# Kernel optimization log

Measured on AMD Instinct MI355X. Metric: run time of the kernel, lower is better.

The kernel has to match this reference:

```python
import jax, jax.numpy as jnp
import numpy as np

B, T, D, K, NF = 4, 1024, 1024, 4, 4
MAXD = 256          # TemporalEncoding max_delta
NC = 32             # ConceptGraph n_concepts
LN_EPS = 1e-5


def setup_inputs() -> dict:
    key = jax.random.key(0)
    ks = jax.random.split(key, 12)
    s = 0.02  # weight init scale
    return {
        "x": jax.random.normal(ks[0], (B, T, D), jnp.float32),
        "routed_tokens": jax.random.normal(ks[1], (B, T, K, D), jnp.float32),
        "sim": jax.random.normal(ks[2], (B, T, K), jnp.float32),
        # per-function logic Linear(3D->D), LayerNorm(D), gate Linear(3D->D)
        "Wl": jax.random.normal(ks[3], (NF, 3 * D, D), jnp.float32) * s,
        "bl": jnp.zeros((NF, D), jnp.float32),
        "ln_g": jnp.ones((NF, D), jnp.float32),
        "ln_b": jnp.zeros((NF, D), jnp.float32),
        "Wg": jax.random.normal(ks[4], (NF, 3 * D, D), jnp.float32) * s,
        "bg": jnp.zeros((NF, D), jnp.float32),
        # fn_selector Linear(D -> NF)
        "Wsel": jax.random.normal(ks[5], (D, NF), jnp.float32) * s,
        "bsel": jnp.zeros((NF,), jnp.float32),
        # temporal embedding table [2*max_delta+1, D]
        "delta_table": jax.random.normal(ks[6], (2 * MAXD + 1, D), jnp.float32) * s,
        # VQ codebook (ConceptGraph.embedding buffer)
        "codebook": jax.random.normal(ks[7], (NC, D), jnp.float32),
        "topk_indices": jax.random.randint(ks[8], (B, T, K), 0, T),
    }


def reference(x, routed_tokens, sim, Wl, bl, ln_g, ln_b, Wg, bg,
              Wsel, bsel, delta_table, codebook, topk_indices):
    Bx, Tx, Dx = x.shape
    Kx = routed_tokens.shape[2]
    N = Bx * Tx

    # temporal encoding: delta = t - topk_index, clamped into table range
    t = jnp.arange(Tx)[None, :, None]
    idx = jnp.clip(t - topk_indices + MAXD, 0, 2 * MAXD)
    de = delta_table[idx].reshape(N, Kx, Dx)            # [N,K,D]

    xf = x.reshape(N, Dx)
    rf = routed_tokens.reshape(N, Kx, Dx)
    sf = sim.reshape(N, Kx)

    tok = jnp.broadcast_to(xf[:, None, :], (N, Kx, Dx))
    comb = jnp.concatenate([tok, rf, de], axis=-1)       # [N,K,3D]

    # all NF reasoning functions at once: logic MLP + GELU + LayerNorm
    h = jnp.einsum('nkc,fcd->fnkd', comb, Wl) + bl[:, None, None, :]
    h = jax.nn.gelu(h, approximate=False)
    mu = jnp.mean(h, axis=-1, keepdims=True)
    var = jnp.var(h, axis=-1, keepdims=True)
    h = (h - mu) / jnp.sqrt(var + LN_EPS)
    h = h * ln_g[:, None, None, :] + ln_b[:, None, None, :]  # [F,N,K,D]

    sw = jax.nn.softmax(sf, axis=-1)                     # [N,K]
    arg = jnp.einsum('nk,fnkd->fnd', sw, h)              # [F,N,D]

    tok_f = jnp.broadcast_to(xf[None], (Wl.shape[0], N, Dx))
    gin = jnp.concatenate([tok_f, arg, arg], axis=-1)    # [F,N,3D]
    gate = jax.nn.sigmoid(jnp.einsum('fnc,fcd->fnd', gin, Wg) + bg[:, None, :])

    fw = jax.nn.softmax(xf @ Wsel + bsel, axis=-1)       # [N,F]
    proposed = jnp.einsum('nf,fnd->nd', fw, arg)
    gsum = jnp.einsum('nf,fnd->nd', fw, gate)
    uf = proposed * gsum                                 # [N,D] updated tokens

    # ConceptGraph VQ (eval: no EMA update): pairwise dist, argmin, gather
    d2 = (jnp.sum(uf * uf, axis=1, keepdims=True)
          - 2.0 * uf @ codebook.T
          + jnp.sum(codebook * codebook, axis=1))        # [N,NC]
    enc = jnp.argmin(d2, axis=1)                         # [N]
    quant = codebook[enc]                                # [N,D]
    out = uf + jax.lax.stop_gradient(quant - uf)         # straight-through
    return out.reshape(Bx, Tx, Dx)
```

## Files before the change

### kernel.cpp

```cpp
#include <hip/hip_runtime.h>
#include <hip/hip_bf16.h>
#include <cmath>


typedef __bf16 bf16x8 __attribute__((ext_vector_type(8)));
typedef float  f32x4  __attribute__((ext_vector_type(4)));

__device__ __forceinline__ float gelu_f(float v) {
    return 0.5f * v * (1.0f + erff(v * 0.7071067811865476f));
}

__device__ __forceinline__ void split8(const float* v, bf16x8& H, bf16x8& L) {
#pragma unroll
    for (int j = 0; j < 8; ++j) {
        float x = v[j];
        __bf16 h = (__bf16)x;
        H[j] = h;
        L[j] = (__bf16)(x - (float)h);
    }
}

#define GLL16(src, dst)                                                        \
    __builtin_amdgcn_global_load_lds(                                          \
        (const __attribute__((address_space(1))) void*)(src),                  \
        (__attribute__((address_space(3))) void*)(dst), 16, 0, 0)

#define SWZ_DECODE()                                                           \
    int bx, by, bz;                                                            \
    {                                                                          \
        const int nx = gridDim.x, ny = gridDim.y;                              \
        const int nwg = nx * ny * (int)gridDim.z;                              \
        const int bid = blockIdx.x + nx * (blockIdx.y + ny * blockIdx.z);      \
        const int q = nwg >> 3;                                                \
        const int rm = (bid & 7) * q + (bid >> 3);                             \
        bx = rm % nx; by = (rm / nx) % ny; bz = rm / (nx * ny);                \
    }

#define STAGE_WRITE()                                                          \
    _Pragma("unroll")                                                          \
    for (int i = 0; i < 4; ++i) {                                              \
        int u = tid + i * 256;                                                 \
        int arow = u >> 3, ag = u & 7;                                         \
        bf16x8 H, L; split8(ra[i], H, L);                                      \
        char* dst = lds + arow * 128 + ((ag ^ (arow & 7)) << 4);               \
        *(bf16x8*)dst = H; *(bf16x8*)(dst + 16384) = L;                        \
    }                                                                          \
    _Pragma("unroll")                                                          \
    for (int i = 0; i < 4; ++i) {                                              \
        int u = tid + i * 256;                                                 \
        int bcol = u & 127, bgu = u >> 7;                                      \
        bf16x8 H, L; split8(rb[i], H, L);                                      \
        char* dst = lds + 32768 + bcol * 128 + ((bgu ^ (bcol & 7)) << 4);      \
        *(bf16x8*)dst = H; *(bf16x8*)(dst + 16384) = L;                        \
    }

#define MFMA64()                                                               \
    _Pragma("unroll")                                                          \
    for (int ks = 0; ks < 2; ++ks) {                                           \
        bf16x8 ah[4], al[4], bh[4], bl_[4];                                    \
        _Pragma("unroll")                                                      \
        for (int mi = 0; mi < 4; ++mi) {                                       \
            const char* pa = lds + (wr + mi * 16 + rl) * 128                   \
                             + (((ks * 4 + g) ^ (rl & 7)) << 4);               \
            ah[mi] = *(const bf16x8*)pa;                                       \
            al[mi] = *(const bf16x8*)(pa + 16384);                             \
        }                                                                      \
        _Pragma("unroll")                                                      \
        for (int ni = 0; ni < 4; ++ni) {                                       \
            const char* pb = lds + 32768 + (wc + ni * 16 + rl) * 128           \
                             + (((ks * 4 + g) ^ (rl & 7)) << 4);               \
            bh[ni]  = *(const bf16x8*)pb;                                      \
            bl_[ni] = *(const bf16x8*)(pb + 16384);                            \
        }                                                                      \
        _Pragma("unroll")                                                      \
        for (int mi = 0; mi < 4; ++mi)                                         \
            _Pragma("unroll")                                                  \
            for (int ni = 0; ni < 4; ++ni) {                                   \
                acc[mi][ni] = __builtin_amdgcn_mfma_f32_16x16x32_bf16(ah[mi], bh[ni],  acc[mi][ni], 0, 0, 0); \
                acc[mi][ni] = __builtin_amdgcn_mfma_f32_16x16x32_bf16(ah[mi], bl_[ni], acc[mi][ni], 0, 0, 0); \
                acc[mi][ni] = __builtin_amdgcn_mfma_f32_16x16x32_bf16(al[mi], bh[ni],  acc[mi][ni], 0, 0, 0); \
            }                                                                  \
    }

__global__ __launch_bounds__(256, 2) void gemm64(
    const float* __restrict__ A, int arowBase, int maxrow,
    const float* __restrict__ B, int kbase,
    float* __restrict__ C, int nkt,
    size_t bStrideZ, size_t cStrideZ, int mrows)
{
    __shared__ __align__(16) char lds[65536];
    const int tid = threadIdx.x, wid = tid >> 6, lane = tid & 63;
    SWZ_DECODE();
    const int bm0 = bx * 128, bn0 = by * 128;
    const float* Bf = B + bz * bStrideZ;
    float* Cp = C + bz * cStrideZ;
    const int wr = (wid >> 1) * 64, wc = (wid & 1) * 64;
    const int g = lane >> 4, rl = lane & 15;

    float ra[4][8], rb[4][8];

#define LOADA64(KC0)                                                           \
    _Pragma("unroll")                                                          \
    for (int i = 0; i < 4; ++i) {                                              \
        int u = tid + i * 256;                                                 \
        int r = arowBase + bm0 + (u >> 3); if (r > maxrow) r = maxrow;         \
        const float* s = A + (size_t)r * 1024 + (KC0) + (u & 7) * 8;           \
        *(float4*)&ra[i][0] = ((const float4*)s)[0];                           \
        *(float4*)&ra[i][4] = ((const float4*)s)[1];                           \
    }
#define LOADB64(KC0)                                                           \
    _Pragma("unroll")                                                          \
    for (int i = 0; i < 4; ++i) {                                              \
        int u = tid + i * 256;                                                 \
        int bcol = bn0 + (u & 127);                                            \
        int k0 = kbase + (KC0) + (u >> 7) * 8;                                 \
        _Pragma("unroll")                                                      \
        for (int j = 0; j < 8; ++j)                                            \
            rb[i][j] = Bf[(size_t)(k0 + j) * 1024 + bcol];                     \
    }

    f32x4 acc[4][4];
    f32x4 zero = {0.f, 0.f, 0.f, 0.f};
#pragma unroll
    for (int i = 0; i < 4; ++i)
#pragma unroll
        for (int j = 0; j < 4; ++j) acc[i][j] = zero;

    LOADA64(0) LOADB64(0)
    for (int kt = 0; kt < nkt; ++kt) {
        STAGE_WRITE()
        __syncthreads();
        if (kt + 1 < nkt) { LOADA64((kt + 1) * 64) LOADB64((kt + 1) * 64) }
        MFMA64()
        __syncthreads();
    }
#undef LOADA64
#undef LOADB64

    const int cg = lane & 15, rg = (lane >> 4) * 4;
#pragma unroll
    for (int mi = 0; mi < 4; ++mi) {
#pragma unroll
        for (int i = 0; i < 4; ++i) {
            int row_out = bm0 + wr + mi * 16 + rg + i;
            if (row_out >= mrows) continue;
#pragma unroll
            for (int ni = 0; ni < 4; ++ni) {
                int col = bn0 + wc + ni * 16 + cg;
                Cp[(size_t)row_out * 1024 + col] = acc[mi][ni][i];
            }
        }
    }
}

__global__ __launch_bounds__(256) void precvt_wg(
    const float* __restrict__ Wg, char* __restrict__ img)
{
    const int u = blockIdx.x * 256 + threadIdx.x;
    const int col = u & 127;
    const int kt  = (u >> 7) & 63;
    const int ct  = (u >> 13) & 7;
    const int f   = u >> 16;
    const int colg = ct * 128 + col;
    const float* Wf = Wg + (size_t)f * 3072 * 1024;
    const bool sum2 = (kt >= 32);

    float vv[32];
#pragma unroll
    for (int j = 0; j < 32; ++j) {
        int k = kt * 32 + j;
        float v = Wf[(size_t)k * 1024 + colg];
        if (sum2) v += Wf[(size_t)(k + 1024) * 1024 + colg];
        vv[j] = v;
    }
    char* tb = img + ((((size_t)f * 8 + ct) * 64) + kt) * 16384;
    const int swz = (col >> 1) & 3;
#pragma unroll
    for (int g = 0; g < 4; ++g) {
        bf16x8 H, L; split8(&vv[g * 8], H, L);
        char* dst = tb + col * 64 + ((g ^ swz) << 4);
        *(bf16x8*)dst = H;
        *(bf16x8*)(dst + 8192) = L;
    }
}

__global__ __launch_bounds__(256, 3) void gate_bimg(
    const float* __restrict__ x, const float* __restrict__ arg,
    const char* __restrict__ img, const float* __restrict__ fw,
    const float* __restrict__ bg, float* __restrict__ g2, int fbase)
{
    __shared__ __align__(16) char lds[49152];
    const int tid = threadIdx.x, wid = tid >> 6, lane = tid & 63;
    SWZ_DECODE();
    const int bm0 = bx * 128, bn0 = by * 128;
    const int z = bz, f = fbase + z;
    const float* argf = arg + (size_t)f * 4096 * 1024;
    const char* Bt = img + (((size_t)f * 8 + by) * 64) * 16384;
    const int wr = (wid >> 1) * 64, wc = (wid & 1) * 64;
    const int g = lane >> 4, rl = lane & 15;
    const int goff = ((g ^ ((rl >> 1) & 3)) << 4);
    const int boff = wid * 4096 + lane * 16;

    float ra[2][8];

#define LOADA_G(KT)                                                            \
    _Pragma("unroll")                                                          \
    for (int i = 0; i < 2; ++i) {                                              \
        int u = tid + i * 256;                                                 \
        int r = bm0 + (u >> 2);                                                \
        int k0 = (KT) * 32 + (u & 3) * 8;                                      \
        const float* s = (k0 < 1024) ? (x + (size_t)r * 1024 + k0)             \
                                     : (argf + (size_t)r * 1024 + (k0 - 1024));\
        *(float4*)&ra[i][0] = ((const float4*)s)[0];                           \
        *(float4*)&ra[i][4] = ((const float4*)s)[1];                           \
    }
#define LOADB_G(KT, BUF)                                                       \
    {                                                                          \
        const char* sb = Bt + (size_t)(KT) * 16384 + boff;                     \
        char* db = lds + 16384 + (BUF) * 16384 + boff;                         \
        GLL16(sb,        db);                                                  \
        GLL16(sb + 1024, db + 1024);                                           \
        GLL16(sb + 2048, db + 2048);                                           \
        GLL16(sb + 3072, db + 3072);                                           \
    }

    f32x4 acc[4][4];
    f32x4 zero = {0.f, 0.f, 0.f, 0.f};
#pragma unroll
    for (int i = 0; i < 4; ++i)
#pragma unroll
        for (int j = 0; j < 4; ++j) acc[i][j] = zero;

    LOADA_G(0)
    LOADB_G(0, 0)
    for (int kt = 0; kt < 64; ++kt) {
        __syncthreads();
#pragma unroll
        for (int i = 0; i < 2; ++i) {
            int u = tid + i * 256;
            int row = u >> 2, ag = u & 3;
            bf16x8 H, L; split8(ra[i], H, L);
            char* dst = lds + row * 64 + ((ag ^ ((row >> 1) & 3)) << 4);
            *(bf16x8*)dst = H;
            *(bf16x8*)(dst + 8192) = L;
        }
        __syncthreads();
        if (kt + 1 < 64) {
            LOADB_G(kt + 1, (kt + 1) & 1)
            LOADA_G(kt + 1)
        }
        {
            const char* LDSA = lds;
            const char* LDSB = lds + 16384 + (kt & 1) * 16384;
            bf16x8 ah[4], al[4], bh[4], bl_[4];
#pragma unroll
            for (int mi = 0; mi < 4; ++mi) {
                const char* pa = LDSA + (wr + mi * 16 + rl) * 64 + goff;
                ah[mi] = *(const bf16x8*)pa;
                al[mi] = *(const bf16x8*)(pa + 8192);
            }
#pragma unroll
            for (int ni = 0; ni < 4; ++ni) {
                const char* pb = LDSB + (wc + ni * 16 + rl) * 64 + goff;
                bh[ni]  = *(const bf16x8*)pb;
                bl_[ni] = *(const bf16x8*)(pb + 8192);
            }
#pragma unroll
            for (int mi = 0; mi < 4; ++mi)
#pragma unroll
                for (int ni = 0; ni < 4; ++ni) {
                    acc[mi][ni] = __builtin_amdgcn_mfma_f32_16x16x32_bf16(ah[mi], bh[ni],  acc[mi][ni], 0, 0, 0);
                    acc[mi][ni] = __builtin_amdgcn_mfma_f32_16x16x32_bf16(ah[mi], bl_[ni], acc[mi][ni], 0, 0, 0);
                    acc[mi][ni] = __builtin_amdgcn_mfma_f32_16x16x32_bf16(al[mi], bh[ni],  acc[mi][ni], 0, 0, 0);
                }
        }
    }
#undef LOADA_G
#undef LOADB_G

    const int cg = lane & 15, rg = (lane >> 4) * 4;
    const bool accum = (fbase > 0);
#pragma unroll
    for (int mi = 0; mi < 4; ++mi) {
#pragma unroll
        for (int i = 0; i < 4; ++i) {
            int row_out = bm0 + wr + mi * 16 + rg + i;
            float fwv = fw[(size_t)row_out * 4 + f];
#pragma unroll
            for (int ni = 0; ni < 4; ++ni) {
                int col = bn0 + wc + ni * 16 + cg;
                float v = acc[mi][ni][i] + bg[f * 1024 + col];
                float s = fwv / (1.0f + expf(-v));
                size_t off = ((size_t)z * 4096 + row_out) * 1024 + col;
                if (accum) g2[off] += s; else g2[off] = s;
            }
        }
    }
}

__global__ __launch_bounds__(256) void fw_kernel(
    const float* __restrict__ x, const float* __restrict__ Wsel,
    const float* __restrict__ bsel, float* __restrict__ fw)
{
    __shared__ float sred[16];
    const int n = blockIdx.x;
    const int tid = threadIdx.x, w = tid >> 6, lane = tid & 63;

    float4 xv = *(const float4*)&x[(size_t)n * 1024 + tid * 4];
    float pf0 = 0, pf1 = 0, pf2 = 0, pf3 = 0;
    const float* wrp = &Wsel[(size_t)tid * 16];
    pf0 += xv.x * wrp[0];  pf1 += xv.x * wrp[1];  pf2 += xv.x * wrp[2];  pf3 += xv.x * wrp[3];
    pf0 += xv.y * wrp[4];  pf1 += xv.y * wrp[5];  pf2 += xv.y * wrp[6];  pf3 += xv.y * wrp[7];
    pf0 += xv.z * wrp[8];  pf1 += xv.z * wrp[9];  pf2 += xv.z * wrp[10]; pf3 += xv.z * wrp[11];
    pf0 += xv.w * wrp[12]; pf1 += xv.w * wrp[13]; pf2 += xv.w * wrp[14]; pf3 += xv.w * wrp[15];
    for (int o = 32; o; o >>= 1) {
        pf0 += __shfl_xor(pf0, o); pf1 += __shfl_xor(pf1, o);
        pf2 += __shfl_xor(pf2, o); pf3 += __shfl_xor(pf3, o);
    }
    if (lane == 0) { sred[w*4+0] = pf0; sred[w*4+1] = pf1; sred[w*4+2] = pf2; sred[w*4+3] = pf3; }
    __syncthreads();
    if (tid == 0) {
        float s0 = sred[0] + sred[4] + sred[8]  + sred[12] + bsel[0];
        float s1 = sred[1] + sred[5] + sred[9]  + sred[13] + bsel[1];
        float s2 = sred[2] + sred[6] + sred[10] + sred[14] + bsel[2];
        float s3 = sred[3] + sred[7] + sred[11] + sred[15] + bsel[3];
        float mx = fmaxf(fmaxf(s0, s1), fmaxf(s2, s3));
        float e0 = expf(s0 - mx), e1 = expf(s1 - mx), e2 = expf(s2 - mx), e3 = expf(s3 - mx);
        float inv = 1.0f / (e0 + e1 + e2 + e3);
        float4 o = { e0 * inv, e1 * inv, e2 * inv, e3 * inv };
        *(float4*)&fw[(size_t)n * 4] = o;
    }
}

__global__ __launch_bounds__(256) void ln_fuse_kernel(
    const float* __restrict__ hpre, const float* __restrict__ de_proj,
    const float* __restrict__ bl, const float* __restrict__ ln_g,
    const float* __restrict__ ln_b, const float* __restrict__ sim,
    const int* __restrict__ topk, float* __restrict__ arg,
    int f, int token_base, const float* __restrict__ xl)
{
    __shared__ float red[4 * 1024];
    const int n = token_base + blockIdx.x;
    const int k = threadIdx.x >> 6, lane = threadIdx.x & 63;
    const float* hrow = hpre + ((size_t)blockIdx.x * 4 + k) * 1024;
    const int t  = n & 1023;
    const int tk = topk[(size_t)n * 4 + k];
    int di = t - tk + 256; di = di < 0 ? 0 : (di > 512 ? 512 : di);
    const float* drow = de_proj + ((size_t)f * 513 + di) * 1024;
    const float* blr = bl + f * 1024;
    const float* gr  = ln_g + f * 1024;
    const float* br  = ln_b + f * 1024;
    const float* xr  = xl + (size_t)n * 1024;

    float4 s4 = *(const float4*)&sim[(size_t)n * 4];
    float smax = fmaxf(fmaxf(s4.x, s4.y), fmaxf(s4.z, s4.w));
    float e0 = expf(s4.x - smax), e1 = expf(s4.y - smax);
    float e2 = expf(s4.z - smax), e3 = expf(s4.w - smax);
    float swk = (k == 0 ? e0 : k == 1 ? e1 : k == 2 ? e2 : e3) / (e0 + e1 + e2 + e3);

    float gv[16];
    float ssum = 0.f;
#pragma unroll
    for (int j = 0; j < 4; ++j) {
        int d4 = lane + j * 64;
        float4 h  = *(const float4*)&hrow[d4 * 4];
        float4 dd = *(const float4*)&drow[d4 * 4];
        float4 bb = *(const float4*)&blr[d4 * 4];
        float4 xv = *(const float4*)&xr[d4 * 4];
        float a0 = gelu_f(h.x + xv.x + dd.x + bb.x);
        float a1 = gelu_f(h.y + xv.y + dd.y + bb.y);
        float a2 = gelu_f(h.z + xv.z + dd.z + bb.z);
        float a3 = gelu_f(h.w + xv.w + dd.w + bb.w);
        gv[j*4+0] = a0; gv[j*4+1] = a1; gv[j*4+2] = a2; gv[j*4+3] = a3;
        ssum += a0 + a1 + a2 + a3;
    }
    for (int o = 32; o; o >>= 1) ssum += __shfl_xor(ssum, o);
    float mu = ssum * 0.0009765625f;
    float vs = 0.f;
#pragma unroll
    for (int i = 0; i < 16; ++i) { float dm = gv[i] - mu; vs += dm * dm; }
    for (int o = 32; o; o >>= 1) vs += __shfl_xor(vs, o);
    float rstd = 1.0f / sqrtf(vs * 0.0009765625f + 1e-5f);
#pragma unroll
    for (int j = 0; j < 4; ++j) {
        int d4 = lane + j * 64;
        float4 g4 = *(const float4*)&gr[d4 * 4];
        float4 b4 = *(const float4*)&br[d4 * 4];
        float4 y;
        y.x = ((gv[j*4+0] - mu) * rstd * g4.x + b4.x) * swk;
        y.y = ((gv[j*4+1] - mu) * rstd * g4.y + b4.y) * swk;
        y.z = ((gv[j*4+2] - mu) * rstd * g4.z + b4.z) * swk;
        y.w = ((gv[j*4+3] - mu) * rstd * g4.w + b4.w) * swk;
        *(float4*)&red[k * 1024 + d4 * 4] = y;
    }
    __syncthreads();
    const int p = threadIdx.x;
    float4 r0 = *(const float4*)&red[0 * 1024 + p * 4];
    float4 r1 = *(const float4*)&red[1 * 1024 + p * 4];
    float4 r2 = *(const float4*)&red[2 * 1024 + p * 4];
    float4 r3 = *(const float4*)&red[3 * 1024 + p * 4];
    float4 o;
    o.x = r0.x + r1.x + r2.x + r3.x;
    o.y = r0.y + r1.y + r2.y + r3.y;
    o.z = r0.z + r1.z + r2.z + r3.z;
    o.w = r0.w + r1.w + r2.w + r3.w;
    *(float4*)&arg[((size_t)f * 4096 + n) * 1024 + p * 4] = o;
}

__global__ __launch_bounds__(256) void final_kernel(
    const float* __restrict__ fw, const float* __restrict__ arg,
    const float* __restrict__ g2, const float* __restrict__ cb,
    float* __restrict__ out)
{
    __shared__ float uf_s[1024];
    __shared__ float score_s[32];
    __shared__ int enc_s;
    const int n = blockIdx.x;
    const int tid = threadIdx.x, w = tid >> 6, lane = tid & 63;

    float4 fwv = *(const float4*)&fw[(size_t)n * 4];
    float fwa[4] = { fwv.x, fwv.y, fwv.z, fwv.w };

    float4 prop = {0, 0, 0, 0};
#pragma unroll
    for (int f = 0; f < 4; ++f) {
        float4 av = *(const float4*)&arg[((size_t)f * 4096 + n) * 1024 + tid * 4];
        prop.x += fwa[f] * av.x; prop.y += fwa[f] * av.y;
        prop.z += fwa[f] * av.z; prop.w += fwa[f] * av.w;
    }
    float4 ga = *(const float4*)&g2[(size_t)n * 1024 + tid * 4];
    float4 gb = *(const float4*)&g2[(size_t)(4096 + n) * 1024 + tid * 4];
    float4 uf;
    uf.x = prop.x * (ga.x + gb.x); uf.y = prop.y * (ga.y + gb.y);
    uf.z = prop.z * (ga.z + gb.z); uf.w = prop.w * (ga.w + gb.w);
    *(float4*)&uf_s[tid * 4] = uf;
    __syncthreads();

#pragma unroll
    for (int cc = 0; cc < 8; ++cc) {
        int c = w * 8 + cc;
        float p = 0.f, q = 0.f;
#pragma unroll
        for (int j = 0; j < 4; ++j) {
            int d4 = lane + j * 64;
            float4 u4 = *(const float4*)&uf_s[d4 * 4];
            float4 c4 = *(const float4*)&cb[(size_t)c * 1024 + d4 * 4];
            p += u4.x * c4.x + u4.y * c4.y + u4.z * c4.z + u4.w * c4.w;
            q += c4.x * c4.x + c4.y * c4.y + c4.z * c4.z + c4.w * c4.w;
        }
        float s = q - 2.0f * p;
        for (int o = 32; o; o >>= 1) s += __shfl_xor(s, o);
        if (lane == 0) score_s[c] = s;
    }
    __syncthreads();
    if (tid < 64) {
        float v; int idx;
        if (lane < 32) { v = score_s[lane]; idx = lane; }
        else           { v = INFINITY;      idx = 1 << 30; }
        for (int o = 16; o; o >>= 1) {
            float ov = __shfl_xor(v, o); int oi = __shfl_xor(idx, o);
            if (ov < v || (ov == v && oi < idx)) { v = ov; idx = oi; }
        }
        if (lane == 0) enc_s = idx;
    }
    __syncthreads();
    const int enc = enc_s;
    float4 o4 = *(const float4*)&cb[(size_t)enc * 1024 + tid * 4];
    *(float4*)&out[(size_t)n * 1024 + tid * 4] = o4;
}

extern "C" void kernel_launch(void* const* d_in, const int* in_sizes, int n_in,
                              void* d_out, int out_size, void* d_ws, size_t ws_size,
                              hipStream_t stream)
{
    const float* x    = (const float*)d_in[0];
    const float* rf   = (const float*)d_in[1];
    const float* sim  = (const float*)d_in[2];
    const float* Wl   = (const float*)d_in[3];
    const float* bl   = (const float*)d_in[4];
    const float* ln_g = (const float*)d_in[5];
    const float* ln_b = (const float*)d_in[6];
    const float* Wg   = (const float*)d_in[7];
    const float* bg   = (const float*)d_in[8];
    const float* Wsel = (const float*)d_in[9];
    const float* bsel = (const float*)d_in[10];
    const float* dtab = (const float*)d_in[11];
    const float* cb   = (const float*)d_in[12];
    const int*   topk = (const int*)d_in[13];
    float* out = (float*)d_out;
    dim3 blk(256);

    const size_t NEED = 142622720ull;
    if (ws_size < NEED) return;
    char* ws = (char*)d_ws;
    float* arg     = (float*)(ws + 0);
    float* de_proj = (float*)(ws + 67108864);
    float* xl2     = (float*)(ws + 75513856);
    float* hbuf    = (float*)(ws + 109068288);
    char*  Wgimg   = ws + 67108864;
    float* g2      = (float*)(ws + 100663296);
    float* fw      = (float*)(ws + 134217728);

    gemm64<<<dim3(5, 8, 4), blk, 0, stream>>>(
        dtab, 0, 512, Wl, 2048, de_proj, 16,
        (size_t)3072 * 1024, (size_t)513 * 1024, 513);

    for (int pair = 0; pair < 2; ++pair) {
        gemm64<<<dim3(32, 8, 2), blk, 0, stream>>>(
            x, 0, 4095, Wl + (size_t)pair * 2 * 3072 * 1024, 0, xl2, 16,
            (size_t)3072 * 1024, (size_t)4096 * 1024, 4096);
        for (int fi = 0; fi < 2; ++fi) {
            int f = pair * 2 + fi;
            const float* Wlf = Wl + (size_t)f * 3072 * 1024;
            const float* xlf = xl2 + (size_t)fi * 4096 * 1024;
            for (int ch = 0; ch < 2; ++ch) {
                gemm64<<<dim3(64, 8, 1), blk, 0, stream>>>(
                    rf, ch * 8192, 16383, Wlf, 1024, hbuf, 16, 0, 0, 8192);
                ln_fuse_kernel<<<2048, blk, 0, stream>>>(
                    hbuf, de_proj, bl, ln_g, ln_b, sim, topk, arg,
                    f, ch * 2048, xlf);
            }
        }
    }

    precvt_wg<<<1024, blk, 0, stream>>>(Wg, Wgimg);

    fw_kernel<<<4096, blk, 0, stream>>>(x, Wsel, bsel, fw);

    gate_bimg<<<dim3(32, 8, 2), blk, 0, stream>>>(x, arg, Wgimg, fw, bg, g2, 0);
    gate_bimg<<<dim3(32, 8, 2), blk, 0, stream>>>(x, arg, Wgimg, fw, bg, g2, 2);

    final_kernel<<<4096, blk, 0, stream>>>(fw, arg, g2, cb, out);
}
```

Measured before the change: 1.094 ms.

## Pre-split routed-token weights into bf16 image and double-buffer LDS in GEMMs

The routed-token GEMM now reads a precomputed hi/lo bf16 image of the Wl middle slice, loaded with global_load_lds, instead of strided fp32 B loads split into bf16 on every tile. The gate GEMM and the new routed GEMM use double-buffered A and B LDS stages with one barrier per k-step. The x projection for all four functions is done in one launch written into the arg buffer, which lets ln_fuse read and overwrite in place. The goal is to cut B-operand conversion work and barrier stalls, at the cost of an extra conversion pass and workspace aliasing between xl and arg.

Result: faster. 1.012 ms (-7.5%).

```diff
diff --git a/kernel.cpp b/kernel.cpp
--- a/kernel.cpp
+++ b/kernel.cpp
@@ -36,12 +36,238 @@
         bx = rm % nx; by = (rm / nx) % ny; bz = rm / (nx * ny);                \
     }
 
-#define STAGE_WRITE()                                                          \
+__global__ __launch_bounds__(256) void precvt_img(
+    const float* __restrict__ W, char* __restrict__ img,
+    int krowBase, int nktLog, int sumFromKt)
+{
+    const int u = blockIdx.x * 256 + threadIdx.x;
+    const int col = u & 127;
+    const int kt  = (u >> 7) & ((1 << nktLog) - 1);
+    const int ct  = (u >> (7 + nktLog)) & 7;
+    const int f   = u >> (10 + nktLog);
+    const int colg = ct * 128 + col;
+    const float* Wf = W + (size_t)f * 3072 * 1024;
+    const bool sum2 = (kt >= sumFromKt);
+
+    float vv[32];
+#pragma unroll
+    for (int j = 0; j < 32; ++j) {
+        int k = krowBase + kt * 32 + j;
+        float v = Wf[(size_t)k * 1024 + colg];
+        if (sum2) v += Wf[(size_t)(k + 1024) * 1024 + colg];
+        vv[j] = v;
+    }
+    char* tb = img + ((((size_t)f * 8 + ct) << nktLog) + kt) * 16384;
+    const int swz = (col >> 1) & 3;
+#pragma unroll
+    for (int g = 0; g < 4; ++g) {
+        bf16x8 H, L; split8(&vv[g * 8], H, L);
+        char* dst = tb + col * 64 + ((g ^ swz) << 4);
+        *(bf16x8*)dst = H;
+        *(bf16x8*)(dst + 8192) = L;
+    }
+}
+
+#define WRITEA_SPLIT(AB)                                                       \
+    {                                                                          \
+        int row = tid >> 2, ag = tid & 3;                                      \
+        bf16x8 H, L; split8(ra[0], H, L);                                      \
+        char* d = (AB) + row * 64 + ((ag ^ ((row >> 1) & 3)) << 4);            \
+        *(bf16x8*)d = H; *(bf16x8*)(d + 8192) = L;                             \
+        int row2 = row + 64;                                                   \
+        split8(ra[1], H, L);                                                   \
+        char* d2 = (AB) + row2 * 64 + ((ag ^ ((row2 >> 1) & 3)) << 4);         \
+        *(bf16x8*)d2 = H; *(bf16x8*)(d2 + 8192) = L;                           \
+    }
+
+#define LOADB_IMG(KT, BB)                                                      \
+    {                                                                          \
+        const char* sb = Bt + (size_t)(KT) * 16384 + boff;                     \
+        char* db = (BB) + boff;                                                \
+        GLL16(sb,        db);                                                  \
+        GLL16(sb + 1024, db + 1024);                                           \
+        GLL16(sb + 2048, db + 2048);                                           \
+        GLL16(sb + 3072, db + 3072);                                           \
+    }
+
+#define MFMA32(AB, BB)                                                         \
+    {                                                                          \
+        bf16x8 ah[4], al[4], bh[4], bl_[4];                                    \
+        _Pragma("unroll")                                                      \
+        for (int mi = 0; mi < 4; ++mi) {                                       \
+            const char* pa = (AB) + (wr + mi * 16 + rl) * 64 + goff;           \
+            ah[mi] = *(const bf16x8*)pa;                                       \
+            al[mi] = *(const bf16x8*)(pa + 8192);                              \
+        }                                                                      \
+        _Pragma("unroll")                                                      \
+        for (int ni = 0; ni < 4; ++ni) {                                       \
+            const char* pb = (BB) + (wc + ni * 16 + rl) * 64 + goff;           \
+            bh[ni]  = *(const bf16x8*)pb;                                      \
+            bl_[ni] = *(const bf16x8*)(pb + 8192);                             \
+        }                                                                      \
+        _Pragma("unroll")                                                      \
+        for (int mi = 0; mi < 4; ++mi)                                         \
+            _Pragma("unroll")                                                  \
+            for (int ni = 0; ni < 4; ++ni) {                                   \
+                acc[mi][ni] = __builtin_amdgcn_mfma_f32_16x16x32_bf16(ah[mi], bh[ni],  acc[mi][ni], 0, 0, 0); \
+                acc[mi][ni] = __builtin_amdgcn_mfma_f32_16x16x32_bf16(ah[mi], bl_[ni], acc[mi][ni], 0, 0, 0); \
+                acc[mi][ni] = __builtin_amdgcn_mfma_f32_16x16x32_bf16(al[mi], bh[ni],  acc[mi][ni], 0, 0, 0); \
+            }                                                                  \
+    }
+
+__global__ __launch_bounds__(256, 2) void himg(
+    const float* __restrict__ rfA, int rowBase,
+    const char* __restrict__ img, int fimg,
+    float* __restrict__ hbuf)
+{
+    __shared__ __align__(16) char lds[65536];
+    const int tid = threadIdx.x, wid = tid >> 6, lane = tid & 63;
+    SWZ_DECODE();
+    (void)bz;
+    const int bm0 = bx * 128, bn0 = by * 128;
+    const char* Bt = img + (size_t)((fimg * 8 + by) << 5) * 16384;
+    const int wr = (wid >> 1) * 64, wc = (wid & 1) * 64;
+    const int g = lane >> 4, rl = lane & 15;
+    const int goff = ((g ^ ((rl >> 1) & 3)) << 4);
+    const int boff = wid * 4096 + lane * 16;
+    char* A0 = lds;            char* A1 = lds + 16384;
+    char* B0 = lds + 32768;    char* B1 = lds + 49152;
+
+    const float* abase = rfA + (size_t)(rowBase + bm0 + (tid >> 2)) * 1024 + (tid & 3) * 8;
+    float ra[2][8];
+#define LOADA_H(KT)                                                            \
+    {                                                                          \
+        const float* s = abase + (KT) * 32;                                    \
+        *(float4*)&ra[0][0] = ((const float4*)s)[0];                           \
+        *(float4*)&ra[0][4] = ((const float4*)s)[1];                           \
+        const float* s2 = s + 64 * 1024;                                       \
+        *(float4*)&ra[1][0] = ((const float4*)s2)[0];                          \
+        *(float4*)&ra[1][4] = ((const float4*)s2)[1];                          \
+    }
+
+    f32x4 acc[4][4];
+    f32x4 zero = {0.f, 0.f, 0.f, 0.f};
+#pragma unroll
+    for (int i = 0; i < 4; ++i)
+#pragma unroll
+        for (int j = 0; j < 4; ++j) acc[i][j] = zero;
+
+    LOADA_H(0)
+    LOADB_IMG(0, B0)
+    WRITEA_SPLIT(A0)
+    LOADA_H(1)
+    __syncthreads();
+    for (int kt = 0; kt < 32; ++kt) {
+        char* Ac = (kt & 1) ? A1 : A0;  char* Bc = (kt & 1) ? B1 : B0;
+        char* An = (kt & 1) ? A0 : A1;  char* Bn = (kt & 1) ? B0 : B1;
+        if (kt < 31) {
+            LOADB_IMG(kt + 1, Bn)
+            WRITEA_SPLIT(An)
+            if (kt < 30) LOADA_H(kt + 2)
+        }
+        MFMA32(Ac, Bc)
+        __syncthreads();
+    }
+#undef LOADA_H
+
+    const int cg = lane & 15, rg = (lane >> 4) * 4;
+#pragma unroll
+    for (int mi = 0; mi < 4; ++mi)
+#pragma unroll
+        for (int i = 0; i < 4; ++i) {
+            int row_out = bm0 + wr + mi * 16 + rg + i;
+#pragma unroll
+            for (int ni = 0; ni < 4; ++ni) {
+                int col = bn0 + wc + ni * 16 + cg;
+                hbuf[(size_t)row_out * 1024 + col] = acc[mi][ni][i];
+            }
+        }
+}
+
+__global__ __launch_bounds__(256, 2) void gate_img(
+    const float* __restrict__ x, const float* __restrict__ arg,
+    const char* __restrict__ img, const float* __restrict__ fw,
+    const float* __restrict__ bg, float* __restrict__ g2, int fbase)
+{
+    __shared__ __align__(16) char lds[65536];
+    const int tid = threadIdx.x, wid = tid >> 6, lane = tid & 63;
+    SWZ_DECODE();
+    const int bm0 = bx * 128, bn0 = by * 128;
+    const int z = bz, f = fbase + z;
+    const float* argf = arg + (size_t)f * 4096 * 1024;
+    const char* Bt = img + (size_t)((f * 8 + by) << 6) * 16384;
+    const int wr = (wid >> 1) * 64, wc = (wid & 1) * 64;
+    const int g = lane >> 4, rl = lane & 15;
+    const int goff = ((g ^ ((rl >> 1) & 3)) << 4);
+    const int boff = wid * 4096 + lane * 16;
+    char* A0 = lds;            char* A1 = lds + 16384;
+    char* B0 = lds + 32768;    char* B1 = lds + 49152;
+
+    const int arow = bm0 + (tid >> 2);
+    const int akc  = (tid & 3) * 8;
+    float ra[2][8];
+#define LOADA_G(KT)                                                            \
+    {                                                                          \
+        int k0 = (KT) * 32 + akc;                                              \
+        const float* base = (k0 < 1024) ? x : (argf - 1024);                   \
+        const float* s  = base + (size_t)arow * 1024 + k0;                     \
+        const float* s2 = base + (size_t)(arow + 64) * 1024 + k0;              \
+        *(float4*)&ra[0][0] = ((const float4*)s)[0];                           \
+        *(float4*)&ra[0][4] = ((const float4*)s)[1];                           \
+        *(float4*)&ra[1][0] = ((const float4*)s2)[0];                          \
+        *(float4*)&ra[1][4] = ((const float4*)s2)[1];                          \
+    }
+
+    f32x4 acc[4][4];
+    f32x4 zero = {0.f, 0.f, 0.f, 0.f};
+#pragma unroll
+    for (int i = 0; i < 4; ++i)
+#pragma unroll
+        for (int j = 0; j < 4; ++j) acc[i][j] = zero;
+
+    LOADA_G(0)
+    LOADB_IMG(0, B0)
+    WRITEA_SPLIT(A0)
+    LOADA_G(1)
+    __syncthreads();
+    for (int kt = 0; kt < 64; ++kt) {
+        char* Ac = (kt & 1) ? A1 : A0;  char* Bc = (kt & 1) ? B1 : B0;
+        char* An = (kt & 1) ? A0 : A1;  char* Bn = (kt & 1) ? B0 : B1;
+        if (kt < 63) {
+            LOADB_IMG(kt + 1, Bn)
+            WRITEA_SPLIT(An)
+            if (kt < 62) LOADA_G(kt + 2)
+        }
+        MFMA32(Ac, Bc)
+        __syncthreads();
+    }
+#undef LOADA_G
+
+    const int cg = lane & 15, rg = (lane >> 4) * 4;
+    const bool accum = (fbase > 0);
+#pragma unroll
+    for (int mi = 0; mi < 4; ++mi)
+#pragma unroll
+        for (int i = 0; i < 4; ++i) {
+            int row_out = bm0 + wr + mi * 16 + rg + i;
+            float fwv = fw[(size_t)row_out * 4 + f];
+#pragma unroll
+            for (int ni = 0; ni < 4; ++ni) {
+                int col = bn0 + wc + ni * 16 + cg;
+                float v = acc[mi][ni][i] + bg[f * 1024 + col];
+                float s = fwv / (1.0f + expf(-v));
+                size_t off = ((size_t)z * 4096 + row_out) * 1024 + col;
+                if (accum) g2[off] += s; else g2[off] = s;
+            }
+        }
+}
+
+#define STAGE_WRITE64()                                                        \
     _Pragma("unroll")                                                          \
     for (int i = 0; i < 4; ++i) {                                              \
         int u = tid + i * 256;                                                 \
         int arow = u >> 3, ag = u & 7;                                         \
-        bf16x8 H, L; split8(ra[i], H, L);                                      \
+        bf16x8 H, L; split8(rav[i], H, L);                                     \
         char* dst = lds + arow * 128 + ((ag ^ (arow & 7)) << 4);               \
         *(bf16x8*)dst = H; *(bf16x8*)(dst + 16384) = L;                        \
     }                                                                          \
@@ -49,7 +275,7 @@
     for (int i = 0; i < 4; ++i) {                                              \
         int u = tid + i * 256;                                                 \
         int bcol = u & 127, bgu = u >> 7;                                      \
-        bf16x8 H, L; split8(rb[i], H, L);                                      \
+        bf16x8 H, L; split8(rbv[i], H, L);                                     \
         char* dst = lds + 32768 + bcol * 128 + ((bgu ^ (bcol & 7)) << 4);      \
         *(bf16x8*)dst = H; *(bf16x8*)(dst + 16384) = L;                        \
     }
@@ -97,7 +323,7 @@
     const int wr = (wid >> 1) * 64, wc = (wid & 1) * 64;
     const int g = lane >> 4, rl = lane & 15;
 
-    float ra[4][8], rb[4][8];
+    float rav[4][8], rbv[4][8];
 
 #define LOADA64(KC0)                                                           \
     _Pragma("unroll")                                                          \
@@ -105,8 +331,8 @@
         int u = tid + i * 256;                                                 \
         int r = arowBase + bm0 + (u >> 3); if (r > maxrow) r = maxrow;         \
         const float* s = A + (size_t)r * 1024 + (KC0) + (u & 7) * 8;           \
-        *(float4*)&ra[i][0] = ((const float4*)s)[0];                           \
-        *(float4*)&ra[i][4] = ((const float4*)s)[1];                           \
+        *(float4*)&rav[i][0] = ((const float4*)s)[0];                          \
+        *(float4*)&rav[i][4] = ((const float4*)s)[1];                          \
     }
 #define LOADB64(KC0)                                                           \
     _Pragma("unroll")                                                          \
@@ -116,7 +342,7 @@
         int k0 = kbase + (KC0) + (u >> 7) * 8;                                 \
         _Pragma("unroll")                                                      \
         for (int j = 0; j < 8; ++j)                                            \
-            rb[i][j] = Bf[(size_t)(k0 + j) * 1024 + bcol];                     \
+            rbv[i][j] = Bf[(size_t)(k0 + j) * 1024 + bcol];                    \
     }
 
     f32x4 acc[4][4];
@@ -128,7 +354,7 @@
 
     LOADA64(0) LOADB64(0)
     for (int kt = 0; kt < nkt; ++kt) {
-        STAGE_WRITE()
+        STAGE_WRITE64()
         __syncthreads();
         if (kt + 1 < nkt) { LOADA64((kt + 1) * 64) LOADB64((kt + 1) * 64) }
         MFMA64()
@@ -139,7 +365,7 @@
 
     const int cg = lane & 15, rg = (lane >> 4) * 4;
 #pragma unroll
-    for (int mi = 0; mi < 4; ++mi) {
+    for (int mi = 0; mi < 4; ++mi)
 #pragma unroll
         for (int i = 0; i < 4; ++i) {
             int row_out = bm0 + wr + mi * 16 + rg + i;
@@ -150,152 +376,6 @@
                 Cp[(size_t)row_out * 1024 + col] = acc[mi][ni][i];
             }
         }
-    }
-}
-
-__global__ __launch_bounds__(256) void precvt_wg(
-    const float* __restrict__ Wg, char* __restrict__ img)
-{
-    const int u = blockIdx.x * 256 + threadIdx.x;
-    const int col = u & 127;
-    const int kt  = (u >> 7) & 63;
-    const int ct  = (u >> 13) & 7;
-    const int f   = u >> 16;
-    const int colg = ct * 128 + col;
-    const float* Wf = Wg + (size_t)f * 3072 * 1024;
-    const bool sum2 = (kt >= 32);
-
-    float vv[32];
-#pragma unroll
-    for (int j = 0; j < 32; ++j) {
-        int k = kt * 32 + j;
-        float v = Wf[(size_t)k * 1024 + colg];
-        if (sum2) v += Wf[(size_t)(k + 1024) * 1024 + colg];
-        vv[j] = v;
-    }
-    char* tb = img + ((((size_t)f * 8 + ct) * 64) + kt) * 16384;
-    const int swz = (col >> 1) & 3;
-#pragma unroll
-    for (int g = 0; g < 4; ++g) {
-        bf16x8 H, L; split8(&vv[g * 8], H, L);
-        char* dst = tb + col * 64 + ((g ^ swz) << 4);
-        *(bf16x8*)dst = H;
-        *(bf16x8*)(dst + 8192) = L;
-    }
-}
-
-__global__ __launch_bounds__(256, 3) void gate_bimg(
-    const float* __restrict__ x, const float* __restrict__ arg,
-    const char* __restrict__ img, const float* __restrict__ fw,
-    const float* __restrict__ bg, float* __restrict__ g2, int fbase)
-{
-    __shared__ __align__(16) char lds[49152];
-    const int tid = threadIdx.x, wid = tid >> 6, lane = tid & 63;
-    SWZ_DECODE();
-    const int bm0 = bx * 128, bn0 = by * 128;
-    const int z = bz, f = fbase + z;
-    const float* argf = arg + (size_t)f * 4096 * 1024;
-    const char* Bt = img + (((size_t)f * 8 + by) * 64) * 16384;
-    const int wr = (wid >> 1) * 64, wc = (wid & 1) * 64;
-    const int g = lane >> 4, rl = lane & 15;
-    const int goff = ((g ^ ((rl >> 1) & 3)) << 4);
-    const int boff = wid * 4096 + lane * 16;
-
-    float ra[2][8];
-
-#define LOADA_G(KT)                                                            \
-    _Pragma("unroll")                                                          \
-    for (int i = 0; i < 2; ++i) {                                              \
-        int u = tid + i * 256;                                                 \
-        int r = bm0 + (u >> 2);                                                \
-        int k0 = (KT) * 32 + (u & 3) * 8;                                      \
-        const float* s = (k0 < 1024) ? (x + (size_t)r * 1024 + k0)             \
-                                     : (argf + (size_t)r * 1024 + (k0 - 1024));\
-        *(float4*)&ra[i][0] = ((const float4*)s)[0];                           \
-        *(float4*)&ra[i][4] = ((const float4*)s)[1];                           \
-    }
-#define LOADB_G(KT, BUF)                                                       \
-    {                                                                          \
-        const char* sb = Bt + (size_t)(KT) * 16384 + boff;                     \
-        char* db = lds + 16384 + (BUF) * 16384 + boff;                         \
-        GLL16(sb,        db);                                                  \
-        GLL16(sb + 1024, db + 1024);                                           \
-        GLL16(sb + 2048, db + 2048);                                           \
-        GLL16(sb + 3072, db + 3072);                                           \
-    }
-
-    f32x4 acc[4][4];
-    f32x4 zero = {0.f, 0.f, 0.f, 0.f};
-#pragma unroll
-    for (int i = 0; i < 4; ++i)
-#pragma unroll
-        for (int j = 0; j < 4; ++j) acc[i][j] = zero;
-
-    LOADA_G(0)
-    LOADB_G(0, 0)
-    for (int kt = 0; kt < 64; ++kt) {
-        __syncthreads();
-#pragma unroll
-        for (int i = 0; i < 2; ++i) {
-            int u = tid + i * 256;
-            int row = u >> 2, ag = u & 3;
-            bf16x8 H, L; split8(ra[i], H, L);
-            char* dst = lds + row * 64 + ((ag ^ ((row >> 1) & 3)) << 4);
-            *(bf16x8*)dst = H;
-            *(bf16x8*)(dst + 8192) = L;
-        }
-        __syncthreads();
-        if (kt + 1 < 64) {
-            LOADB_G(kt + 1, (kt + 1) & 1)
-            LOADA_G(kt + 1)
-        }
-        {
-            const char* LDSA = lds;
-            const char* LDSB = lds + 16384 + (kt & 1) * 16384;
-            bf16x8 ah[4], al[4], bh[4], bl_[4];
-#pragma unroll
-            for (int mi = 0; mi < 4; ++mi) {
-                const char* pa = LDSA + (wr + mi * 16 + rl) * 64 + goff;
-                ah[mi] = *(const bf16x8*)pa;
-                al[mi] = *(const bf16x8*)(pa + 8192);
-            }
-#pragma unroll
-            for (int ni = 0; ni < 4; ++ni) {
-                const char* pb = LDSB + (wc + ni * 16 + rl) * 64 + goff;
-                bh[ni]  = *(const bf16x8*)pb;
-                bl_[ni] = *(const bf16x8*)(pb + 8192);
-            }
-#pragma unroll
-            for (int mi = 0; mi < 4; ++mi)
-#pragma unroll
-                for (int ni = 0; ni < 4; ++ni) {
-                    acc[mi][ni] = __builtin_amdgcn_mfma_f32_16x16x32_bf16(ah[mi], bh[ni],  acc[mi][ni], 0, 0, 0);
-                    acc[mi][ni] = __builtin_amdgcn_mfma_f32_16x16x32_bf16(ah[mi], bl_[ni], acc[mi][ni], 0, 0, 0);
-                    acc[mi][ni] = __builtin_amdgcn_mfma_f32_16x16x32_bf16(al[mi], bh[ni],  acc[mi][ni], 0, 0, 0);
-                }
-        }
-    }
-#undef LOADA_G
-#undef LOADB_G
-
-    const int cg = lane & 15, rg = (lane >> 4) * 4;
-    const bool accum = (fbase > 0);
-#pragma unroll
-    for (int mi = 0; mi < 4; ++mi) {
-#pragma unroll
-        for (int i = 0; i < 4; ++i) {
-            int row_out = bm0 + wr + mi * 16 + rg + i;
-            float fwv = fw[(size_t)row_out * 4 + f];
-#pragma unroll
-            for (int ni = 0; ni < 4; ++ni) {
-                int col = bn0 + wc + ni * 16 + cg;
-                float v = acc[mi][ni][i] + bg[f * 1024 + col];
-                float s = fwv / (1.0f + expf(-v));
-                size_t off = ((size_t)z * 4096 + row_out) * 1024 + col;
-                if (accum) g2[off] += s; else g2[off] = s;
-            }
-        }
-    }
 }
 
 __global__ __launch_bounds__(256) void fw_kernel(
@@ -336,8 +416,8 @@
     const float* __restrict__ hpre, const float* __restrict__ de_proj,
     const float* __restrict__ bl, const float* __restrict__ ln_g,
     const float* __restrict__ ln_b, const float* __restrict__ sim,
-    const int* __restrict__ topk, float* __restrict__ arg,
-    int f, int token_base, const float* __restrict__ xl)
+    const int* __restrict__ topk, float* arg,
+    int f, int token_base, const float* xl)
 {
     __shared__ float red[4 * 1024];
     const int n = token_base + blockIdx.x;
@@ -495,8 +575,8 @@
     char* ws = (char*)d_ws;
     float* arg     = (float*)(ws + 0);
     float* de_proj = (float*)(ws + 67108864);
-    float* xl2     = (float*)(ws + 75513856);
-    float* hbuf    = (float*)(ws + 109068288);
+    float* hbuf    = (float*)(ws + 75513856);
+    char*  Wl1img  = ws + 109068288;
     char*  Wgimg   = ws + 67108864;
     float* g2      = (float*)(ws + 100663296);
     float* fw      = (float*)(ws + 134217728);
@@ -505,30 +585,29 @@
         dtab, 0, 512, Wl, 2048, de_proj, 16,
         (size_t)3072 * 1024, (size_t)513 * 1024, 513);
 
-    for (int pair = 0; pair < 2; ++pair) {
-        gemm64<<<dim3(32, 8, 2), blk, 0, stream>>>(
-            x, 0, 4095, Wl + (size_t)pair * 2 * 3072 * 1024, 0, xl2, 16,
-            (size_t)3072 * 1024, (size_t)4096 * 1024, 4096);
-        for (int fi = 0; fi < 2; ++fi) {
-            int f = pair * 2 + fi;
-            const float* Wlf = Wl + (size_t)f * 3072 * 1024;
-            const float* xlf = xl2 + (size_t)fi * 4096 * 1024;
-            for (int ch = 0; ch < 2; ++ch) {
-                gemm64<<<dim3(64, 8, 1), blk, 0, stream>>>(
-                    rf, ch * 8192, 16383, Wlf, 1024, hbuf, 16, 0, 0, 8192);
-                ln_fuse_kernel<<<2048, blk, 0, stream>>>(
-                    hbuf, de_proj, bl, ln_g, ln_b, sim, topk, arg,
-                    f, ch * 2048, xlf);
-            }
-        }
-    }
-
-    precvt_wg<<<1024, blk, 0, stream>>>(Wg, Wgimg);
+    gemm64<<<dim3(32, 8, 4), blk, 0, stream>>>(
+        x, 0, 4095, Wl, 0, arg, 16,
+        (size_t)3072 * 1024, (size_t)4096 * 1024, 4096);
+
+    precvt_img<<<512, blk, 0, stream>>>(Wl, Wl1img, 1024, 5, 99);
+
+    for (int f = 0; f < 4; ++f) {
+        const float* xlf = arg + (size_t)f * 4096 * 1024;
+        for (int ch = 0; ch < 2; ++ch) {
+            himg<<<dim3(64, 8), blk, 0, stream>>>(
+                rf, ch * 8192, Wl1img, f, hbuf);
+            ln_fuse_kernel<<<2048, blk, 0, stream>>>(
+                hbuf, de_proj, bl, ln_g, ln_b, sim, topk, arg,
+                f, ch * 2048, xlf);
+        }
+    }
+
+    precvt_img<<<1024, blk, 0, stream>>>(Wg, Wgimg, 0, 6, 32);
 
     fw_kernel<<<4096, blk, 0, stream>>>(x, Wsel, bsel, fw);
 
-    gate_bimg<<<dim3(32, 8, 2), blk, 0, stream>>>(x, arg, Wgimg, fw, bg, g2, 0);
-    gate_bimg<<<dim3(32, 8, 2), blk, 0, stream>>>(x, arg, Wgimg, fw, bg, g2, 2);
+    gate_img<<<dim3(32, 8, 2), blk, 0, stream>>>(x, arg, Wgimg, fw, bg, g2, 0);
+    gate_img<<<dim3(32, 8, 2), blk, 0, stream>>>(x, arg, Wgimg, fw, bg, g2, 2);
 
     final_kernel<<<4096, blk, 0, stream>>>(fw, arg, g2, cb, out);
 }
```
